# Kernel tuning notes

Measured on AMD Instinct MI355X. Metric: run time of the kernel, lower is better.

The kernel has to match this reference:

```python
import jax, jax.numpy as jnp
import numpy as np

NEG_INF = -1e30  # stand-in for -inf that is safe under fp16/bf16 softmax


def setup_inputs() -> dict:
    key = jax.random.key(0)
    k1, k2, k3, k4 = jax.random.split(key, 4)
    B, T, C, H = 4, 4096, 1024, 64
    x = jax.random.normal(k1, (B, T, C), dtype=jnp.float32)
    Wq = jax.random.normal(k2, (C, H), dtype=jnp.float32) * (C ** -0.5)
    Wk = jax.random.normal(k3, (C, H), dtype=jnp.float32) * (C ** -0.5)
    Wv = jax.random.normal(k4, (C, H), dtype=jnp.float32) * (C ** -0.5)
    return {"x": x, "Wq": Wq, "Wk": Wk, "Wv": Wv}


def reference(x, Wq, Wk, Wv):
    # x: [B,T,C]; Wq/Wk/Wv: [C,H]
    q = jnp.einsum('btc,ch->bth', x, Wq)
    k = jnp.einsum('btc,ch->bth', x, Wk)
    v = jnp.einsum('btc,ch->bth', x, Wv)
    # NOTE: original module applies NO 1/sqrt(head_size) scaling — faithful here.
    wei = jnp.einsum('bqh,bkh->bqk', q, k)  # [B,T,T]
    T = x.shape[1]
    causal = jnp.tril(jnp.ones((T, T), dtype=bool))
    wei = jnp.where(causal, wei, NEG_INF)
    wei = jax.nn.softmax(wei, axis=-1)
    # dropout: eval-mode identity
    out = jnp.einsum('bqk,bkh->bqh', wei, v)  # [B,T,H]
    return out
```

## Files before the change

kernel.cpp:

```cpp
#include <hip/hip_runtime.h>
#include <hip/hip_fp16.h>


typedef __attribute__((ext_vector_type(8))) short bf16x8;
typedef __attribute__((ext_vector_type(8))) unsigned short u16x8;
typedef __attribute__((ext_vector_type(4))) float f32x4;

__device__ __forceinline__ unsigned short f2bf(float f) {
  unsigned u = __float_as_uint(f);
  u += 0x7fffu + ((u >> 16) & 1u);
  return (unsigned short)(u >> 16);
}
__device__ __forceinline__ float bf2f(unsigned short s) {
  return __uint_as_float(((unsigned)s) << 16);
}
__device__ __forceinline__ unsigned cvt_pk_bf16(float lo, float hi) {
  unsigned r;
  asm("v_cvt_pk_bf16_f32 %0, %1, %2" : "=v"(r) : "v"(lo), "v"(hi));
  return r;
}
__device__ __forceinline__ void gload_lds16(const void* g, void* l) {
  __builtin_amdgcn_global_load_lds(
      (const __attribute__((address_space(1))) unsigned int*)g,
      (__attribute__((address_space(3))) unsigned int*)l, 16, 0, 0);
}
#define KSWZ(row, colb) ((((row) * 128) + (colb)) ^ (((row) & 7) << 4))

__global__ __launch_bounds__(256) void wsplit_kernel(
    const float* __restrict__ Wq, const float* __restrict__ Wk,
    const float* __restrict__ Wv,
    unsigned short* __restrict__ Wth, unsigned short* __restrict__ Wtl) {
  const int fl = blockIdx.x * 256 + threadIdx.x;
  const int lane = fl & 63;
  const int rest = fl >> 6;
  const int nf = rest % 12;
  const int ksq = rest / 12;
  const int n = nf * 16 + (lane & 15);
  const int k0 = ksq * 32 + (lane >> 4) * 8;
  const float* wp = (n < 64) ? Wq : ((n < 128) ? Wk : Wv);
  const int h = n & 63;
  u16x8 hi, lo;
#pragma unroll
  for (int j = 0; j < 8; ++j) {
    float v = wp[(size_t)(k0 + j) * 64 + h];
    unsigned short hh = f2bf(v);
    hi[j] = hh;
    lo[j] = f2bf(v - bf2f(hh));
  }
  const size_t base = (size_t)fl * 8;
  *reinterpret_cast<u16x8*>(&Wth[base]) = hi;
  *reinterpret_cast<u16x8*>(&Wtl[base]) = lo;
}

__global__ __launch_bounds__(256) void proj_mfma_kernel(
    const float* __restrict__ x,
    const unsigned short* __restrict__ Wth, const unsigned short* __restrict__ Wtl,
    unsigned short* __restrict__ qh, unsigned short* __restrict__ ql,
    unsigned short* __restrict__ kh, unsigned short* __restrict__ kl,
    unsigned short* __restrict__ vt) {
  __shared__ unsigned short Ah[2][32][72];
  __shared__ unsigned short Al[2][32][72];
  const int tid = threadIdx.x;
  const int w = tid >> 6;
  const int lane = tid & 63;
  const int l16 = lane & 15;
  const int g = lane >> 4;
  const int row0 = blockIdx.x * 32;
  const int sr = tid >> 3;
  const int sc = (tid & 7) * 8;

  f32x4 acc[2][3];
#pragma unroll
  for (int m = 0; m < 2; ++m)
#pragma unroll
    for (int f = 0; f < 3; ++f) {
      f32x4 z = {0.f, 0.f, 0.f, 0.f};
      acc[m][f] = z;
    }

  const size_t xrow = (size_t)(row0 + sr) * 1024 + sc;
  {
    const float4 xa = *reinterpret_cast<const float4*>(&x[xrow]);
    const float4 xb = *reinterpret_cast<const float4*>(&x[xrow + 4]);
    float v[8] = {xa.x, xa.y, xa.z, xa.w, xb.x, xb.y, xb.z, xb.w};
    u16x8 hv, lv;
#pragma unroll
    for (int j = 0; j < 8; ++j) {
      unsigned short hh = f2bf(v[j]);
      hv[j] = hh;
      lv[j] = f2bf(v[j] - bf2f(hh));
    }
    *reinterpret_cast<u16x8*>(&Ah[0][sr][sc]) = hv;
    *reinterpret_cast<u16x8*>(&Al[0][sr][sc]) = lv;
  }

  for (int step = 0; step < 16; ++step) {
    __syncthreads();
    float4 na, nb;
    if (step < 15) {
      na = *reinterpret_cast<const float4*>(&x[xrow + (size_t)(step + 1) * 64]);
      nb = *reinterpret_cast<const float4*>(&x[xrow + (size_t)(step + 1) * 64 + 4]);
    }
    const int cur = step & 1;
#pragma unroll
    for (int ks = 0; ks < 2; ++ks) {
      bf16x8 bh[3], bl[3];
#pragma unroll
      for (int f = 0; f < 3; ++f) {
        const size_t off = ((size_t)(step * 2 + ks) * 12 + (w * 3 + f)) * 512 + lane * 8;
        bh[f] = *reinterpret_cast<const bf16x8*>(&Wth[off]);
        bl[f] = *reinterpret_cast<const bf16x8*>(&Wtl[off]);
      }
      bf16x8 ah[2], al[2];
#pragma unroll
      for (int m = 0; m < 2; ++m) {
        const int ro = m * 16 + l16;
        const int co = ks * 32 + g * 8;
        ah[m] = *reinterpret_cast<const bf16x8*>(&Ah[cur][ro][co]);
        al[m] = *reinterpret_cast<const bf16x8*>(&Al[cur][ro][co]);
      }
#pragma unroll
      for (int m = 0; m < 2; ++m)
#pragma unroll
        for (int f = 0; f < 3; ++f) {
          acc[m][f] = __builtin_amdgcn_mfma_f32_16x16x32_bf16(ah[m], bh[f], acc[m][f], 0, 0, 0);
          acc[m][f] = __builtin_amdgcn_mfma_f32_16x16x32_bf16(ah[m], bl[f], acc[m][f], 0, 0, 0);
          acc[m][f] = __builtin_amdgcn_mfma_f32_16x16x32_bf16(al[m], bh[f], acc[m][f], 0, 0, 0);
        }
    }
    if (step < 15) {
      float v[8] = {na.x, na.y, na.z, na.w, nb.x, nb.y, nb.z, nb.w};
      u16x8 hv, lv;
#pragma unroll
      for (int j = 0; j < 8; ++j) {
        unsigned short hh = f2bf(v[j]);
        hv[j] = hh;
        lv[j] = f2bf(v[j] - bf2f(hh));
      }
      *reinterpret_cast<u16x8*>(&Ah[cur ^ 1][sr][sc]) = hv;
      *reinterpret_cast<u16x8*>(&Al[cur ^ 1][sr][sc]) = lv;
    }
  }

  const int b = row0 >> 12;
  const int tbase = row0 & 4095;
#pragma unroll
  for (int m = 0; m < 2; ++m)
#pragma unroll
    for (int f = 0; f < 3; ++f) {
      const int nn = w * 48 + f * 16;
      if (nn < 64) {
        const int h = nn + l16;
#pragma unroll
        for (int j = 0; j < 4; ++j) {
          const int row = row0 + m * 16 + 4 * g + j;
          const float val = acc[m][f][j];
          const unsigned short hi = f2bf(val);
          qh[(size_t)row * 64 + h] = hi;
          ql[(size_t)row * 64 + h] = f2bf(val - bf2f(hi));
        }
      } else if (nn < 128) {
        const int h = nn - 64 + l16;
#pragma unroll
        for (int j = 0; j < 4; ++j) {
          const int row = row0 + m * 16 + 4 * g + j;
          const float val = acc[m][f][j];
          const unsigned short hi = f2bf(val);
          kh[(size_t)row * 64 + h] = hi;
          kl[(size_t)row * 64 + h] = f2bf(val - bf2f(hi));
        }
      } else {
        const int h = nn - 128 + l16;
        ushort4 pv;
        pv.x = f2bf(acc[m][f][0]);
        pv.y = f2bf(acc[m][f][1]);
        pv.z = f2bf(acc[m][f][2]);
        pv.w = f2bf(acc[m][f][3]);
        const size_t a = ((size_t)b * 64 + h) * 4096 + tbase + m * 16 + 4 * g;
        *reinterpret_cast<ushort4*>(&vt[a]) = pv;
      }
    }
}

template <int PT>
__global__ __launch_bounds__(256) void attn_part_block_kernel(
    const unsigned short* __restrict__ qh, const unsigned short* __restrict__ ql,
    const unsigned short* __restrict__ kh, const unsigned short* __restrict__ kl,
    const unsigned short* __restrict__ vt,
    __half* __restrict__ OP, float* __restrict__ ML) {
  constexpr int NU_B = (PT == 2) ? 528 : 272;
  __shared__ __align__(16) unsigned short Khs[4096];
  __shared__ __align__(16) unsigned short Kls[4096];
  __shared__ __align__(16) unsigned short Vs[4096];
  __shared__ __align__(16) unsigned short pbuf[4][2][16][88];
  const int tid = threadIdx.x;
  const int w = tid >> 6;
  const int lane = tid & 63;
  const int l16 = lane & 15;
  const int g = lane >> 4;

  const int bx = blockIdx.x;
  const int xc = bx & 7;
  const int b = xc >> 1;
  const int s = 2 * (bx >> 3) + (xc & 1);
  int k = 0;
  if (PT == 2) { while (s >= ((k + 1) * (k + 2)) / 2) ++k; }
  else         { while (s >= ((k + 2) * (k + 2)) / 4) ++k; }
  const int j4 = k;
  const int p = s - ((PT == 2) ? (j4 * (j4 + 1)) / 2 : ((j4 + 1) * (j4 + 1)) / 4);
  const int ntiles = 2 * j4 + 2;
  const int t0 = p * PT;
  const int t1 = min(ntiles, t0 + PT);
  const int q0 = j4 * 128 + w * 32;
  const size_t rowbase = (size_t)b * 4096;

  bf16x8 q0hf[2], q0lf[2], q1hf[2], q1lf[2];
#pragma unroll
  for (int ss = 0; ss < 2; ++ss) {
    size_t a0 = (rowbase + q0 + l16) * 64 + ss * 32 + g * 8;
    q0hf[ss] = *reinterpret_cast<const bf16x8*>(&qh[a0]);
    q0lf[ss] = *reinterpret_cast<const bf16x8*>(&ql[a0]);
    size_t a1 = a0 + 16 * 64;
    q1hf[ss] = *reinterpret_cast<const bf16x8*>(&qh[a1]);
    q1lf[ss] = *reinterpret_cast<const bf16x8*>(&ql[a1]);
  }

  f32x4 o0[4], o1[4];
#pragma unroll
  for (int hb = 0; hb < 4; ++hb) {
    f32x4 z = {0.f, 0.f, 0.f, 0.f};
    o0[hb] = z;
    o1[hb] = z;
  }
  float m0 = -1e30f, l0 = 0.f, m1 = -1e30f, l1 = 0.f;

  for (int t = t0; t < t1; ++t) {
    const int kv0 = t * 64;
#pragma unroll
    for (int half = 0; half < 2; ++half) {
      const int te = half * 256 + w * 64 + lane;
      const int r = te >> 3;
      const int c8 = (te & 7) ^ (r & 7);
      const int ldsoff = half * 4096 + w * 1024 + lane * 16;
      gload_lds16(&kh[(rowbase + kv0 + r) * 64 + c8 * 8], (char*)Khs + ldsoff);
      gload_lds16(&kl[(rowbase + kv0 + r) * 64 + c8 * 8], (char*)Kls + ldsoff);
      gload_lds16(&vt[((size_t)b * 64 + r) * 4096 + kv0 + c8 * 8], (char*)Vs + ldsoff);
    }
    __syncthreads();

    f32x4 s0[4], s1[4];
#pragma unroll
    for (int kb = 0; kb < 4; ++kb) {
      bf16x8 khf[2], klf[2];
#pragma unroll
      for (int ss = 0; ss < 2; ++ss) {
        const int row = kb * 16 + l16;
        const int colb = ss * 64 + g * 16;
        khf[ss] = *reinterpret_cast<const bf16x8*>((const char*)Khs + KSWZ(row, colb));
        klf[ss] = *reinterpret_cast<const bf16x8*>((const char*)Kls + KSWZ(row, colb));
      }
      f32x4 a0 = {0.f, 0.f, 0.f, 0.f};
      f32x4 a1 = {0.f, 0.f, 0.f, 0.f};
#pragma unroll
      for (int ss = 0; ss < 2; ++ss) {
        a0 = __builtin_amdgcn_mfma_f32_16x16x32_bf16(khf[ss], q0hf[ss], a0, 0, 0, 0);
        a0 = __builtin_amdgcn_mfma_f32_16x16x32_bf16(khf[ss], q0lf[ss], a0, 0, 0, 0);
        a0 = __builtin_amdgcn_mfma_f32_16x16x32_bf16(klf[ss], q0hf[ss], a0, 0, 0, 0);
        a1 = __builtin_amdgcn_mfma_f32_16x16x32_bf16(khf[ss], q1hf[ss], a1, 0, 0, 0);
        a1 = __builtin_amdgcn_mfma_f32_16x16x32_bf16(khf[ss], q1lf[ss], a1, 0, 0, 0);
        a1 = __builtin_amdgcn_mfma_f32_16x16x32_bf16(klf[ss], q1hf[ss], a1, 0, 0, 0);
      }
      s0[kb] = a0;
      s1[kb] = a1;
    }
    if (kv0 + 63 > q0) {
#pragma unroll
      for (int kb = 0; kb < 4; ++kb)
#pragma unroll
        for (int jj = 0; jj < 4; ++jj) {
          const int kvg = kv0 + kb * 16 + 4 * g + jj;
          if (kvg > q0 + l16) s0[kb][jj] = -1e30f;
          if (kvg > q0 + 16 + l16) s1[kb][jj] = -1e30f;
        }
    }
    float rm0 = s0[0][0], rm1 = s1[0][0];
#pragma unroll
    for (int kb = 0; kb < 4; ++kb) {
      float c0 = fmaxf(fmaxf(s0[kb][0], s0[kb][1]), fmaxf(s0[kb][2], s0[kb][3]));
      float c1 = fmaxf(fmaxf(s1[kb][0], s1[kb][1]), fmaxf(s1[kb][2], s1[kb][3]));
      rm0 = fmaxf(rm0, c0);
      rm1 = fmaxf(rm1, c1);
    }
    rm0 = fmaxf(rm0, __shfl_xor(rm0, 16));
    rm0 = fmaxf(rm0, __shfl_xor(rm0, 32));
    rm1 = fmaxf(rm1, __shfl_xor(rm1, 16));
    rm1 = fmaxf(rm1, __shfl_xor(rm1, 32));
    const float mn0 = fmaxf(m0, rm0);
    const float mn1 = fmaxf(m1, rm1);
    const float al0 = __expf(m0 - mn0);
    const float al1 = __expf(m1 - mn1);
    float ps0 = 0.f, ps1 = 0.f;
#pragma unroll
    for (int kb = 0; kb < 4; ++kb)
#pragma unroll
      for (int jj = 0; jj < 4; ++jj) {
        const float e0 = __expf(s0[kb][jj] - mn0);
        const float e1 = __expf(s1[kb][jj] - mn1);
        s0[kb][jj] = e0;
        s1[kb][jj] = e1;
        ps0 += e0;
        ps1 += e1;
      }
    ps0 += __shfl_xor(ps0, 16);
    ps0 += __shfl_xor(ps0, 32);
    ps1 += __shfl_xor(ps1, 16);
    ps1 += __shfl_xor(ps1, 32);
    l0 = l0 * al0 + ps0;
    m0 = mn0;
    l1 = l1 * al1 + ps1;
    m1 = mn1;
#pragma unroll
    for (int kb = 0; kb < 4; ++kb) {
      *reinterpret_cast<unsigned*>(&pbuf[w][0][l16][kb * 16 + 4 * g]) =
          cvt_pk_bf16(s0[kb][0], s0[kb][1]);
      *reinterpret_cast<unsigned*>(&pbuf[w][0][l16][kb * 16 + 4 * g + 2]) =
          cvt_pk_bf16(s0[kb][2], s0[kb][3]);
      *reinterpret_cast<unsigned*>(&pbuf[w][1][l16][kb * 16 + 4 * g]) =
          cvt_pk_bf16(s1[kb][0], s1[kb][1]);
      *reinterpret_cast<unsigned*>(&pbuf[w][1][l16][kb * 16 + 4 * g + 2]) =
          cvt_pk_bf16(s1[kb][2], s1[kb][3]);
    }
    bf16x8 vf[2][4];
#pragma unroll
    for (int ks = 0; ks < 2; ++ks)
#pragma unroll
      for (int hb = 0; hb < 4; ++hb) {
        const int row = hb * 16 + l16;
        const int colb = ks * 64 + g * 16;
        vf[ks][hb] = *reinterpret_cast<const bf16x8*>((const char*)Vs + KSWZ(row, colb));
      }
#pragma unroll
    for (int jj = 0; jj < 4; ++jj) {
      const int srcr = 4 * g + jj;
      const float a0r = __shfl(al0, srcr);
      const float a1r = __shfl(al1, srcr);
#pragma unroll
      for (int hb = 0; hb < 4; ++hb) {
        o0[hb][jj] *= a0r;
        o1[hb][jj] *= a1r;
      }
    }
    asm volatile("s_waitcnt lgkmcnt(0)" ::: "memory");
#pragma unroll
    for (int ks = 0; ks < 2; ++ks) {
      bf16x8 pa0 = *reinterpret_cast<const bf16x8*>(&pbuf[w][0][l16][ks * 32 + g * 8]);
      bf16x8 pa1 = *reinterpret_cast<const bf16x8*>(&pbuf[w][1][l16][ks * 32 + g * 8]);
#pragma unroll
      for (int hb = 0; hb < 4; ++hb) {
        o0[hb] = __builtin_amdgcn_mfma_f32_16x16x32_bf16(pa0, vf[ks][hb], o0[hb], 0, 0, 0);
        o1[hb] = __builtin_amdgcn_mfma_f32_16x16x32_bf16(pa1, vf[ks][hb], o1[hb], 0, 0, 0);
      }
    }
    __syncthreads();
  }

  const size_t u = (size_t)b * NU_B + s;
  __half* op = OP + u * 8192 + (size_t)w * 32 * 64;
#pragma unroll
  for (int jj = 0; jj < 4; ++jj) {
    const int srcr = 4 * g + jj;
    const float l0r = __shfl(l0, srcr);
    const float l1r = __shfl(l1, srcr);
#pragma unroll
    for (int hb = 0; hb < 4; ++hb) {
      op[(4 * g + jj) * 64 + hb * 16 + l16] = __float2half(o0[hb][jj] / l0r);
      op[(16 + 4 * g + jj) * 64 + hb * 16 + l16] = __float2half(o1[hb][jj] / l1r);
    }
  }
  float* ml = ML + u * 256 + w * 64;
  if (lane < 16) {
    ml[lane] = m0;
    ml[32 + lane] = l0;
  } else if (lane < 32) {
    ml[lane] = m1;
    ml[32 + lane] = l1;
  }
}

template <int PT>
__global__ __launch_bounds__(256) void attn_combine_kernel(
    const __half* __restrict__ OP, const float* __restrict__ ML,
    float* __restrict__ out) {
  constexpr int NU_B = (PT == 2) ? 528 : 272;
  const int tid = threadIdx.x;
  const int w = tid >> 6;
  const int lane = tid & 63;
  const int rid = blockIdx.x * 4 + w;
  const int b = rid >> 12;
  const int rr = rid & 4095;
  const int j4 = rr >> 7;
  const int local = rr & 127;
  const int nparts = (2 * j4 + 2 + PT - 1) / PT;
  const int prefix = (PT == 2) ? (j4 * (j4 + 1)) / 2 : ((j4 + 1) * (j4 + 1)) / 4;
  const size_t base = (size_t)b * NU_B + prefix;
  const int wv = local >> 5;
  const int tile = (local >> 4) & 1;
  const int rowin = local & 15;
  const int mi = wv * 64 + tile * 16 + rowin;

  float M = -1e30f;
  for (int p = 0; p < nparts; ++p) M = fmaxf(M, ML[(base + p) * 256 + mi]);
  float wsum = 0.f, acc = 0.f;
  for (int p = 0; p < nparts; ++p) {
    const float m = ML[(base + p) * 256 + mi];
    const float l = ML[(base + p) * 256 + 32 + mi];
    const float wg = l * __expf(m - M);
    wsum += wg;
    acc += wg * __half2float(OP[(base + p) * 8192 + (size_t)local * 64 + lane]);
  }
  out[(size_t)rid * 64 + lane] = acc / wsum;
}

extern "C" void kernel_launch(void* const* d_in, const int* in_sizes, int n_in,
                              void* d_out, int out_size, void* d_ws, size_t ws_size,
                              hipStream_t stream) {
  const float* x  = (const float*)d_in[0];
  const float* Wq = (const float*)d_in[1];
  const float* Wk = (const float*)d_in[2];
  const float* Wv = (const float*)d_in[3];
  float* out = (float*)d_out;

  const size_t N = (size_t)4 * 4096 * 64;
  const size_t WN = (size_t)192 * 1024;
  unsigned short* qh = (unsigned short*)d_ws;
  unsigned short* ql = qh + N;
  unsigned short* kh = ql + N;
  unsigned short* kl = kh + N;
  unsigned short* vt = kl + N;
  unsigned short* Wth = vt + N;
  unsigned short* Wtl = Wth + WN;
  __half* OP = (__half*)(Wtl + WN);
  const size_t base_need = (5 * N + 2 * WN) * 2;

  const size_t NU2 = 4 * 528, NU4 = 4 * 272;
  const size_t need2 = base_need + NU2 * 8192 * 2 + NU2 * 256 * 4;
  const size_t need4 = base_need + NU4 * 8192 * 2 + NU4 * 256 * 4;

  wsplit_kernel<<<dim3(96), dim3(256), 0, stream>>>(Wq, Wk, Wv, Wth, Wtl);
  proj_mfma_kernel<<<dim3(512), dim3(256), 0, stream>>>(x, Wth, Wtl, qh, ql, kh, kl, vt);
  if (ws_size >= need2) {
    float* ML = (float*)(OP + NU2 * 8192);
    attn_part_block_kernel<2><<<dim3(NU2), dim3(256), 0, stream>>>(qh, ql, kh, kl, vt, OP, ML);
    attn_combine_kernel<2><<<dim3(4096), dim3(256), 0, stream>>>(OP, ML, out);
  } else {
    float* ML = (float*)(OP + NU4 * 8192);
    attn_part_block_kernel<4><<<dim3(NU4), dim3(256), 0, stream>>>(qh, ql, kh, kl, vt, OP, ML);
    attn_combine_kernel<4><<<dim3(4096), dim3(256), 0, stream>>>(OP, ML, out);
  }
}
```

Baseline: 110.3 us.

## Use lazy online-softmax rescaling, hoist V fragment loads, default to four-tile partitions

New measurement: 96.64 us. 12.4% less time.

```diff
diff --git a/kernel.cpp b/kernel.cpp
--- a/kernel.cpp
+++ b/kernel.cpp
@@ -182,13 +182,12 @@
     }
 }
 
-template <int PT>
+template <int PT, int NU_B>
 __global__ __launch_bounds__(256) void attn_part_block_kernel(
     const unsigned short* __restrict__ qh, const unsigned short* __restrict__ ql,
     const unsigned short* __restrict__ kh, const unsigned short* __restrict__ kl,
     const unsigned short* __restrict__ vt,
     __half* __restrict__ OP, float* __restrict__ ML) {
-  constexpr int NU_B = (PT == 2) ? 528 : 272;
   __shared__ __align__(16) unsigned short Khs[4096];
   __shared__ __align__(16) unsigned short Kls[4096];
   __shared__ __align__(16) unsigned short Vs[4096];
@@ -203,11 +202,15 @@
   const int xc = bx & 7;
   const int b = xc >> 1;
   const int s = 2 * (bx >> 3) + (xc & 1);
-  int k = 0;
-  if (PT == 2) { while (s >= ((k + 1) * (k + 2)) / 2) ++k; }
-  else         { while (s >= ((k + 2) * (k + 2)) / 4) ++k; }
+  int k = 0, pref = 0;
+  for (;;) {
+    const int np = (2 * k + 2 + PT - 1) / PT;
+    if (s < pref + np) break;
+    pref += np;
+    ++k;
+  }
   const int j4 = k;
-  const int p = s - ((PT == 2) ? (j4 * (j4 + 1)) / 2 : ((j4 + 1) * (j4 + 1)) / 4);
+  const int p = s - pref;
   const int ntiles = 2 * j4 + 2;
   const int t0 = p * PT;
   const int t1 = min(ntiles, t0 + PT);
@@ -273,6 +276,15 @@
       s0[kb] = a0;
       s1[kb] = a1;
     }
+    bf16x8 vf[2][4];
+#pragma unroll
+    for (int ks = 0; ks < 2; ++ks)
+#pragma unroll
+      for (int hb = 0; hb < 4; ++hb) {
+        const int row = hb * 16 + l16;
+        const int colb = ks * 64 + g * 16;
+        vf[ks][hb] = *reinterpret_cast<const bf16x8*>((const char*)Vs + KSWZ(row, colb));
+      }
     if (kv0 + 63 > q0) {
 #pragma unroll
       for (int kb = 0; kb < 4; ++kb)
@@ -295,17 +307,19 @@
     rm0 = fmaxf(rm0, __shfl_xor(rm0, 32));
     rm1 = fmaxf(rm1, __shfl_xor(rm1, 16));
     rm1 = fmaxf(rm1, __shfl_xor(rm1, 32));
-    const float mn0 = fmaxf(m0, rm0);
-    const float mn1 = fmaxf(m1, rm1);
-    const float al0 = __expf(m0 - mn0);
-    const float al1 = __expf(m1 - mn1);
+    const bool r0 = !__all(rm0 - m0 <= 8.f);
+    const bool r1 = !__all(rm1 - m1 <= 8.f);
+    const float mu0 = r0 ? fmaxf(m0, rm0) : m0;
+    const float mu1 = r1 ? fmaxf(m1, rm1) : m1;
+    const float al0 = r0 ? __expf(m0 - mu0) : 1.f;
+    const float al1 = r1 ? __expf(m1 - mu1) : 1.f;
     float ps0 = 0.f, ps1 = 0.f;
 #pragma unroll
     for (int kb = 0; kb < 4; ++kb)
 #pragma unroll
       for (int jj = 0; jj < 4; ++jj) {
-        const float e0 = __expf(s0[kb][jj] - mn0);
-        const float e1 = __expf(s1[kb][jj] - mn1);
+        const float e0 = __expf(s0[kb][jj] - mu0);
+        const float e1 = __expf(s1[kb][jj] - mu1);
         s0[kb][jj] = e0;
         s1[kb][jj] = e1;
         ps0 += e0;
@@ -316,9 +330,9 @@
     ps1 += __shfl_xor(ps1, 16);
     ps1 += __shfl_xor(ps1, 32);
     l0 = l0 * al0 + ps0;
-    m0 = mn0;
+    m0 = mu0;
     l1 = l1 * al1 + ps1;
-    m1 = mn1;
+    m1 = mu1;
 #pragma unroll
     for (int kb = 0; kb < 4; ++kb) {
       *reinterpret_cast<unsigned*>(&pbuf[w][0][l16][kb * 16 + 4 * g]) =
@@ -330,24 +344,20 @@
       *reinterpret_cast<unsigned*>(&pbuf[w][1][l16][kb * 16 + 4 * g + 2]) =
           cvt_pk_bf16(s1[kb][2], s1[kb][3]);
     }
-    bf16x8 vf[2][4];
-#pragma unroll
-    for (int ks = 0; ks < 2; ++ks)
-#pragma unroll
-      for (int hb = 0; hb < 4; ++hb) {
-        const int row = hb * 16 + l16;
-        const int colb = ks * 64 + g * 16;
-        vf[ks][hb] = *reinterpret_cast<const bf16x8*>((const char*)Vs + KSWZ(row, colb));
-      }
-#pragma unroll
-    for (int jj = 0; jj < 4; ++jj) {
-      const int srcr = 4 * g + jj;
-      const float a0r = __shfl(al0, srcr);
-      const float a1r = __shfl(al1, srcr);
-#pragma unroll
-      for (int hb = 0; hb < 4; ++hb) {
-        o0[hb][jj] *= a0r;
-        o1[hb][jj] *= a1r;
+    if (r0) {
+#pragma unroll
+      for (int jj = 0; jj < 4; ++jj) {
+        const float a0r = __shfl(al0, 4 * g + jj);
+#pragma unroll
+        for (int hb = 0; hb < 4; ++hb) o0[hb][jj] *= a0r;
+      }
+    }
+    if (r1) {
+#pragma unroll
+      for (int jj = 0; jj < 4; ++jj) {
+        const float a1r = __shfl(al1, 4 * g + jj);
+#pragma unroll
+        for (int hb = 0; hb < 4; ++hb) o1[hb][jj] *= a1r;
       }
     }
     asm volatile("s_waitcnt lgkmcnt(0)" ::: "memory");
@@ -387,11 +397,10 @@
   }
 }
 
-template <int PT>
+template <int PT, int NU_B>
 __global__ __launch_bounds__(256) void attn_combine_kernel(
     const __half* __restrict__ OP, const float* __restrict__ ML,
     float* __restrict__ out) {
-  constexpr int NU_B = (PT == 2) ? 528 : 272;
   const int tid = threadIdx.x;
   const int w = tid >> 6;
   const int lane = tid & 63;
@@ -401,7 +410,8 @@
   const int j4 = rr >> 7;
   const int local = rr & 127;
   const int nparts = (2 * j4 + 2 + PT - 1) / PT;
-  const int prefix = (PT == 2) ? (j4 * (j4 + 1)) / 2 : ((j4 + 1) * (j4 + 1)) / 4;
+  int prefix = 0;
+  for (int k = 0; k < j4; ++k) prefix += (2 * k + 2 + PT - 1) / PT;
   const size_t base = (size_t)b * NU_B + prefix;
   const int wv = local >> 5;
   const int tile = (local >> 4) & 1;
@@ -442,19 +452,19 @@
   __half* OP = (__half*)(Wtl + WN);
   const size_t base_need = (5 * N + 2 * WN) * 2;
 
-  const size_t NU2 = 4 * 528, NU4 = 4 * 272;
-  const size_t need2 = base_need + NU2 * 8192 * 2 + NU2 * 256 * 4;
+  const size_t NU4 = 4 * 272, NU8 = 4 * 144;
   const size_t need4 = base_need + NU4 * 8192 * 2 + NU4 * 256 * 4;
+  const size_t need8 = base_need + NU8 * 8192 * 2 + NU8 * 256 * 4;
 
   wsplit_kernel<<<dim3(96), dim3(256), 0, stream>>>(Wq, Wk, Wv, Wth, Wtl);
   proj_mfma_kernel<<<dim3(512), dim3(256), 0, stream>>>(x, Wth, Wtl, qh, ql, kh, kl, vt);
-  if (ws_size >= need2) {
-    float* ML = (float*)(OP + NU2 * 8192);
-    attn_part_block_kernel<2><<<dim3(NU2), dim3(256), 0, stream>>>(qh, ql, kh, kl, vt, OP, ML);
-    attn_combine_kernel<2><<<dim3(4096), dim3(256), 0, stream>>>(OP, ML, out);
+  if (ws_size >= need4) {
+    float* ML = (float*)(OP + NU4 * 8192);
+    attn_part_block_kernel<4, 272><<<dim3(NU4), dim3(256), 0, stream>>>(qh, ql, kh, kl, vt, OP, ML);
+    attn_combine_kernel<4, 272><<<dim3(4096), dim3(256), 0, stream>>>(OP, ML, out);
   } else {
-    float* ML = (float*)(OP + NU4 * 8192);
-    attn_part_block_kernel<4><<<dim3(NU4), dim3(256), 0, stream>>>(qh, ql, kh, kl, vt, OP, ML);
-    attn_combine_kernel<4><<<dim3(4096), dim3(256), 0, stream>>>(OP, ML, out);
-  }
-}
+    float* ML = (float*)(OP + NU8 * 8192);
+    attn_part_block_kernel<8, 144><<<dim3(NU8), dim3(256), 0, stream>>>(qh, ql, kh, kl, vt, OP, ML);
+    attn_combine_kernel<8, 144><<<dim3(4096), dim3(256), 0, stream>>>(OP, ML, out);
+  }
+}
```
